# Kernel tuning notes

Hardware: AMD Instinct MI355X
Metric: run time of the kernel (lower is better)

The kernel has to match this reference:

```python
import jax, jax.numpy as jnp
import numpy as np
import math

SUB = 0.8  # subset fraction (init kwarg)


def _capsule_weighted_average(x):
    # x: [B, I, O, D, H, W]; norm-weighted average over input caps (dim 1)
    n = jnp.linalg.norm(x, axis=3, keepdims=True)  # [B, I, O, 1, H, W]
    return (n * x).sum(axis=1) / n.sum(axis=1)      # [B, O, D, H, W]


def setup_inputs() -> dict:
    key = jax.random.key(0)
    # [B, input_caps, output_caps, pose_dim, H, W, kh, kw]
    x = jax.random.normal(key, (8, 32, 32, 8, 14, 14, 3, 3), dtype=jnp.float32)
    return {"x": x}


def reference(x):
    B, I, O, D, H, W = x.shape[:6]
    x = x.reshape(B, I, O, D, H, W, -1)             # flatten kernel positions -> K
    # norm-weighted average over the K kernel positions
    xn = jnp.linalg.norm(x, axis=3, keepdims=True)  # [B, I, O, 1, H, W, K]
    x = (xn * x).sum(axis=-1) / xn.sum(axis=-1)     # [B, I, O, D, H, W]

    v = _capsule_weighted_average(x)                # [B, O, D, H, W]

    # 'mse' metric: negative dot product between consensus v and each input capsule
    losses = -(v[:, None] * x).sum(axis=3)          # [B, I, O, H, W]
    subset_size = math.ceil(SUB * I)
    # kthvalue (k-th smallest) along input-caps dim
    thr = jnp.sort(losses, axis=1)[:, subset_size - 1:subset_size]  # [B, 1, O, H, W]
    choose = (losses <= thr).astype(x.dtype)[:, :, :, None]          # [B, I, O, 1, H, W]
    x = x * jax.lax.stop_gradient(choose)

    return _capsule_weighted_average(x)             # [B, O, D, H, W]
```

## Files before the change

kernel.cpp:

```cpp
#include <hip/hip_runtime.h>

#define B 8
#define I 32
#define O 32
#define D 8
#define H 14
#define W 14
#define K 9
#define WK (W*K)
#define DSTRIDE (H*W*K)
#define OSTRIDE (D*H*W*K)
#define ISTRIDE (O*D*H*W*K)
#define BSTRIDE ((size_t)I*ISTRIDE)
#define SUBSET 26

__global__ __launch_bounds__(448) void caps_route_kernel(const float* __restrict__ x,
                                                         float* __restrict__ out) {
    const int bid = blockIdx.x;
    const int h = bid % H;
    const int o = (bid / H) % O;
    const int b = bid / (H * O);
    const int t = threadIdx.x;
    const int i = t / W;
    const int w = t - i * W;

    __shared__ float ys[I][D][W];
    __shared__ float ns_s[I][W];
    __shared__ float ls_s[I][W];
    __shared__ float vsh[D][W];
    __shared__ float thr_s[W];

    const float* xp = x + (size_t)b * BSTRIDE + (size_t)i * ISTRIDE
                        + (size_t)o * OSTRIDE + (size_t)h * WK + (size_t)w * K;

    float xv[D][K];
    #pragma unroll
    for (int d = 0; d < D; ++d) {
        #pragma unroll
        for (int k = 0; k < K; ++k) {
            xv[d][k] = xp[d * DSTRIDE + k];
        }
    }

    float nk[K];
    float den = 0.f;
    #pragma unroll
    for (int k = 0; k < K; ++k) {
        float s = 0.f;
        #pragma unroll
        for (int d = 0; d < D; ++d) { float v = xv[d][k]; s += v * v; }
        nk[k] = sqrtf(s);
        den += nk[k];
    }
    const float inv_den = 1.f / den;

    float y[D];
    float s2 = 0.f;
    #pragma unroll
    for (int d = 0; d < D; ++d) {
        float num = 0.f;
        #pragma unroll
        for (int k = 0; k < K; ++k) num += nk[k] * xv[d][k];
        y[d] = num * inv_den;
        ys[i][d][w] = y[d];
        s2 += y[d] * y[d];
    }
    const float nsv = sqrtf(s2);
    ns_s[i][w] = nsv;
    __syncthreads();

    if (t < D * W) {
        const int d = t / W, w2 = t - (t / W) * W;
        float num = 0.f, dn = 0.f;
        #pragma unroll
        for (int j = 0; j < I; ++j) {
            float nv = ns_s[j][w2];
            num += nv * ys[j][d][w2];
            dn += nv;
        }
        vsh[d][w2] = num / dn;
    }
    __syncthreads();

    float lv = 0.f;
    #pragma unroll
    for (int d = 0; d < D; ++d) lv += vsh[d][w] * y[d];
    lv = -lv;
    ls_s[i][w] = lv;
    __syncthreads();

    int rank = 0;
    #pragma unroll
    for (int j = 0; j < I; ++j) {
        float lj = ls_s[j][w];
        rank += (lj < lv || (lj == lv && j < i)) ? 1 : 0;
    }
    if (rank == SUBSET - 1) thr_s[w] = lv;
    __syncthreads();

    if (t < D * W) {
        const int d = t / W, w2 = t - (t / W) * W;
        const float tw = thr_s[w2];
        float num = 0.f, dn = 0.f;
        #pragma unroll
        for (int j = 0; j < I; ++j) {
            float m  = (ls_s[j][w2] <= tw) ? 1.f : 0.f;
            float nv = m * ns_s[j][w2];
            num += nv * ys[j][d][w2];
            dn  += nv;
        }
        out[(((size_t)b * O + o) * D + d) * (H * W) + h * W + w2] = num / dn;
    }
}

extern "C" void kernel_launch(void* const* d_in, const int* in_sizes, int n_in,
                              void* d_out, int out_size, void* d_ws, size_t ws_size,
                              hipStream_t stream) {
    const float* x = (const float*)d_in[0];
    float* out = (float*)d_out;
    dim3 grid(B * O * H);
    dim3 block(I * W);
    caps_route_kernel<<<grid, block, 0, stream>>>(x, out);
}
```

Before: 607.1 us.

## Split each thread's work across w-pairs and d-halves for float2 vector loads

Each thread now loads two adjacent w positions (18 contiguous floats) for half of the pose dims using float2 loads, instead of 9 floats for all 8 dims. Partial norms and dot products are combined across the thread pair with xor shuffles. The aim is wider, more coalesced global loads of the dominant input read. In exchange it adds shuffle traffic and relies on 8-byte alignment, which holds because w0*K is even.

Measured after the change: 636.2 us. 1.05x slower.

```diff
diff --git a/kernel.cpp b/kernel.cpp
--- a/kernel.cpp
+++ b/kernel.cpp
@@ -21,8 +21,14 @@
     const int o = (bid / H) % O;
     const int b = bid / (H * O);
     const int t = threadIdx.x;
-    const int i = t / W;
-    const int w = t - i * W;
+
+    const int i  = t / W;
+    const int r  = t - i * W;
+    const int wp = r >> 1;
+    const int dh = r & 1;
+    const int w0 = wp << 1;
+    const int wm = w0 + dh;
+    const int d0 = dh << 2;
 
     __shared__ float ys[I][D][W];
     __shared__ float ns_s[I][W];
@@ -31,42 +37,64 @@
     __shared__ float thr_s[W];
 
     const float* xp = x + (size_t)b * BSTRIDE + (size_t)i * ISTRIDE
-                        + (size_t)o * OSTRIDE + (size_t)h * WK + (size_t)w * K;
+                        + (size_t)o * OSTRIDE + (size_t)d0 * DSTRIDE
+                        + (size_t)h * WK + (size_t)w0 * K;
 
-    float xv[D][K];
+    float xv[4][18];
     #pragma unroll
-    for (int d = 0; d < D; ++d) {
+    for (int dd = 0; dd < 4; ++dd) {
+        const float2* p2 = reinterpret_cast<const float2*>(xp + dd * DSTRIDE);
         #pragma unroll
-        for (int k = 0; k < K; ++k) {
-            xv[d][k] = xp[d * DSTRIDE + k];
+        for (int e = 0; e < 9; ++e) {
+            float2 v = p2[e];
+            xv[dd][2*e]   = v.x;
+            xv[dd][2*e+1] = v.y;
         }
     }
 
-    float nk[K];
-    float den = 0.f;
+    float nk[2][K];
+    float den[2];
     #pragma unroll
-    for (int k = 0; k < K; ++k) {
-        float s = 0.f;
+    for (int ww = 0; ww < 2; ++ww) {
+        den[ww] = 0.f;
         #pragma unroll
-        for (int d = 0; d < D; ++d) { float v = xv[d][k]; s += v * v; }
-        nk[k] = sqrtf(s);
-        den += nk[k];
+        for (int k = 0; k < K; ++k) {
+            float s = 0.f;
+            #pragma unroll
+            for (int dd = 0; dd < 4; ++dd) {
+                float v = xv[dd][ww * K + k];
+                s += v * v;
+            }
+            s += __shfl_xor(s, 1);
+            float n = sqrtf(s);
+            nk[ww][k] = n;
+            den[ww] += n;
+        }
     }
-    const float inv_den = 1.f / den;
+    const float invden0 = 1.f / den[0];
+    const float invden1 = 1.f / den[1];
 
-    float y[D];
-    float s2 = 0.f;
+    float y[4][2];
+    float s2p0 = 0.f, s2p1 = 0.f;
     #pragma unroll
-    for (int d = 0; d < D; ++d) {
-        float num = 0.f;
+    for (int dd = 0; dd < 4; ++dd) {
+        float num0 = 0.f, num1 = 0.f;
         #pragma unroll
-        for (int k = 0; k < K; ++k) num += nk[k] * xv[d][k];
-        y[d] = num * inv_den;
-        ys[i][d][w] = y[d];
-        s2 += y[d] * y[d];
+        for (int k = 0; k < K; ++k) {
+            num0 += nk[0][k] * xv[dd][k];
+            num1 += nk[1][k] * xv[dd][K + k];
+        }
+        const float y0 = num0 * invden0;
+        const float y1 = num1 * invden1;
+        y[dd][0] = y0;
+        y[dd][1] = y1;
+        s2p0 += y0 * y0;
+        s2p1 += y1 * y1;
+        *reinterpret_cast<float2*>(&ys[i][d0 + dd][w0]) = make_float2(y0, y1);
     }
-    const float nsv = sqrtf(s2);
-    ns_s[i][w] = nsv;
+    const float s2t0 = s2p0 + __shfl_xor(s2p0, 1);
+    const float s2t1 = s2p1 + __shfl_xor(s2p1, 1);
+    ns_s[i][wm] = sqrtf(dh ? s2t1 : s2t0);
     __syncthreads();
 
     if (t < D * W) {
@@ -82,20 +110,25 @@
     }
     __syncthreads();
 
-    float lv = 0.f;
+    float lp0 = 0.f, lp1 = 0.f;
     #pragma unroll
-    for (int d = 0; d < D; ++d) lv += vsh[d][w] * y[d];
-    lv = -lv;
-    ls_s[i][w] = lv;
+    for (int dd = 0; dd < 4; ++dd) {
+        lp0 += vsh[d0 + dd][w0]     * y[dd][0];
+        lp1 += vsh[d0 + dd][w0 + 1] * y[dd][1];
+    }
+    const float l0 = lp0 + __shfl_xor(lp0, 1);
+    const float l1 = lp1 + __shfl_xor(lp1, 1);
+    const float lv = -(dh ? l1 : l0);
+    ls_s[i][wm] = lv;
     __syncthreads();
 
     int rank = 0;
     #pragma unroll
     for (int j = 0; j < I; ++j) {
-        float lj = ls_s[j][w];
+        float lj = ls_s[j][wm];
         rank += (lj < lv || (lj == lv && j < i)) ? 1 : 0;
     }
-    if (rank == SUBSET - 1) thr_s[w] = lv;
+    if (rank == SUBSET - 1) thr_s[wm] = lv;
     __syncthreads();
 
     if (t < D * W) {
```
